# Kernel tuning notes

Measured on AMD Instinct MI355X. Metric: run time of the kernel, lower is better.

The kernel has to match this reference:

```python
import jax, jax.numpy as jnp
import numpy as np

GROUPS = 8   # channels // group_size with group_size=8 for C=64
EPS = 1e-5


def group_norm_qc(x0, x1, gamma, beta):
    """LatticeGroupNorm: stats computed jointly over both cosets per (batch, group)."""
    B, C, H, W = x0.shape
    g = GROUPS
    xg = jnp.concatenate([x0.reshape(B, g, -1), x1.reshape(B, g, -1)], axis=-1)
    mean = xg.mean(axis=-1).reshape(B, g, 1, 1, 1)
    var = xg.var(axis=-1).reshape(B, g, 1, 1, 1)
    inv = jax.lax.rsqrt(var + EPS)
    ga = gamma[None, :, None, None]
    be = beta[None, :, None, None]

    def norm(x):
        xr = x.reshape(B, g, C // g, H, W)
        return ((xr - mean) * inv).reshape(B, C, H, W) * ga + be

    return norm(x0), norm(x1)


def qc_conv(x0, x1, w_center, w_corner, bias):
    """Quincunx LatticePad+LatticeConvolution with stencil
    [(0,0),(2,0),(0,2),(2,2),(1,1)], center (1,1).
    w_center: [O,I] tap (1,1) (same-coset 1x1).
    w_corner: [O,I,2,2] taps (0,0),(2,0),(0,2),(2,2) (cross-coset 2x2).
    Pad keeps output cosets the same size as inputs ('same' lattice conv)."""
    dn = ('NCHW', 'OIHW', 'NCHW')

    def c1(x):
        return jnp.einsum('oi,bihw->bohw', w_center, x)

    def c2(x, pad):
        return jax.lax.conv_general_dilated(x, w_corner, (1, 1), pad,
                                            dimension_numbers=dn)

    b = bias[None, :, None, None]
    # coset0 output gathers coset1 at (i-1+a, j-1+b) -> pad top/left
    out0 = c1(x0) + c2(x1, ((1, 0), (1, 0))) + b
    # coset1 output gathers coset0 at (i+a, j+b) -> pad bottom/right
    out1 = c1(x1) + c2(x0, ((0, 1), (0, 1))) + b
    return out0, out1


def setup_inputs() -> dict:
    key = jax.random.key(0)
    ks = jax.random.split(key, 10)
    B, C, H, W = 2, 64, 256, 256
    s = 0.05
    return {
        'x0': jax.random.normal(ks[0], (B, C, H, W), jnp.float32),
        'x1': jax.random.normal(ks[1], (B, C, H, W), jnp.float32),
        'g1': jnp.ones((C,), jnp.float32),
        'b1': jnp.zeros((C,), jnp.float32),
        'w1_center': jax.random.normal(ks[2], (C, C), jnp.float32) * s,
        'w1_corner': jax.random.normal(ks[3], (C, C, 2, 2), jnp.float32) * s,
        'bias1': jax.random.normal(ks[4], (C,), jnp.float32) * s,
        'g2': jnp.ones((C,), jnp.float32),
        'b2': jnp.zeros((C,), jnp.float32),
        'w2_center': jax.random.normal(ks[5], (C, C), jnp.float32) * s,
        'w2_corner': jax.random.normal(ks[6], (C, C, 2, 2), jnp.float32) * s,
        'bias2': jax.random.normal(ks[7], (C,), jnp.float32) * s,
        'w_skip': jax.random.normal(ks[8], (C, C), jnp.float32) * s,
        'bias_skip': jax.random.normal(ks[9], (C,), jnp.float32) * s,
        'g_skip': jnp.ones((C,), jnp.float32),
        'beta_skip': jnp.zeros((C,), jnp.float32),
    }


def reference(x0, x1, g1, b1, w1_center, w1_corner, bias1,
              g2, b2, w2_center, w2_corner, bias2,
              w_skip, bias_skip, g_skip, beta_skip):
    # conv path: GN -> ReLU -> pad+conv -> GN -> ReLU -> pad+conv
    h0, h1 = group_norm_qc(x0, x1, g1, b1)
    h0, h1 = jax.nn.relu(h0), jax.nn.relu(h1)
    h0, h1 = qc_conv(h0, h1, w1_center, w1_corner, bias1)
    h0, h1 = group_norm_qc(h0, h1, g2, b2)
    h0, h1 = jax.nn.relu(h0), jax.nn.relu(h1)
    h0, h1 = qc_conv(h0, h1, w2_center, w2_corner, bias2)
    # skip path: 1x1 lattice conv (stencil [(0,0)]) -> GN
    bsk = bias_skip[None, :, None, None]
    s0 = jnp.einsum('oi,bihw->bohw', w_skip, x0) + bsk
    s1 = jnp.einsum('oi,bihw->bohw', w_skip, x1) + bsk
    s0, s1 = group_norm_qc(s0, s1, g_skip, beta_skip)
    # residual add; stack the two cosets as leading axis for a single output
    return jnp.stack([h0 + s0, h1 + s1])
```

## Files before the change

### kernel.cpp

```cpp
#include <hip/hip_runtime.h>

typedef __attribute__((ext_vector_type(8))) __bf16 bf16x8;
typedef __attribute__((ext_vector_type(4))) __bf16 bf16x4;
typedef __attribute__((ext_vector_type(4))) float f32x4;

#define MFMA16(a,b,c) __builtin_amdgcn_mfma_f32_16x16x32_bf16(a,b,c,0,0,0)

static constexpr int HW = 65536;
static constexpr int WD = 256;
static constexpr int NB = 2;
static constexpr double INV_N = 1.0 / 1048576.0;
static constexpr float EPSV = 1e-5f;

static constexpr size_t OFF_P1  = 0;
static constexpr size_t OFF_P2  = 131072;
static constexpr size_t OFF_A1  = 200704;
static constexpr size_t OFF_A2  = OFF_A1 + 40960;
static constexpr size_t OFF_XT  = OFF_A2 + 40960;
static constexpr size_t SZ_T    = (size_t)2 * NB * HW * 64 * 2;
static constexpr size_t OFF_S   = OFF_XT + SZ_T;
static constexpr size_t OFF_H   = OFF_S + SZ_T;

__global__ __launch_bounds__(256) void K1(
    const float* __restrict__ x0, const float* __restrict__ x1,
    const float* __restrict__ wskip, const float* __restrict__ bskip,
    const float* __restrict__ wc1, const float* __restrict__ wk1,
    const float* __restrict__ wc2, const float* __restrict__ wk2,
    __bf16* __restrict__ xt, __bf16* __restrict__ sout,
    __bf16* __restrict__ A1, __bf16* __restrict__ A2, float* __restrict__ p1) {
  const int bx = blockIdx.x;
  const int t = threadIdx.x;

  if (bx >= 1024) {
    const int stage = bx - 1024;
    const float* wc = stage ? wc2 : wc1;
    const float* wk = stage ? wk2 : wk1;
    __bf16* A = stage ? A2 : A1;
    for (int idx = t; idx < 64 * 320; idx += 256) {
      int o = idx / 320, k = idx - o * 320;
      float v;
      if (k < 64) v = wc[o * 64 + k];
      else {
        int tp = (k - 64) >> 6;
        int c = k & 63;
        v = wk[(o * 64 + c) * 4 + tp];
      }
      A[idx] = (__bf16)v;
    }
    return;
  }

  const int row = bx & 255;
  const int b   = (bx >> 8) & 1;
  const int co  = bx >> 9;
  const float* x = co ? x1 : x0;
  __shared__ __attribute__((aligned(16))) __bf16 tile[256 * 72];
  __shared__ float redp[256];
  __shared__ float reds[32];
  const int wv = t >> 6, lane = t & 63;

  const float* xbase = x + (size_t)b * 64 * HW + (size_t)row * WD + t;
  __bf16* xtbase = xt + (((size_t)(co * NB + b) * HW) + (size_t)row * WD + t) * 64;

  float gsum[8], gsq[8];
#pragma unroll
  for (int g = 0; g < 8; ++g) { gsum[g] = 0.f; gsq[g] = 0.f; }
#pragma unroll
  for (int cg = 0; cg < 8; ++cg) {
    float f[8];
#pragma unroll
    for (int j = 0; j < 8; ++j) f[j] = xbase[(size_t)(cg * 8 + j) * HW];
    bf16x8 v;
#pragma unroll
    for (int j = 0; j < 8; ++j) {
      v[j] = (__bf16)f[j];
      gsum[cg] += f[j];
      gsq[cg] = fmaf(f[j], f[j], gsq[cg]);
    }
    *(bf16x8*)&tile[t * 72 + cg * 8] = v;
    *(bf16x8*)&xtbase[cg * 8] = v;
  }
#pragma unroll
  for (int g = 0; g < 8; ++g) {
#pragma unroll
    for (int m = 1; m < 16; m <<= 1) {
      gsum[g] += __shfl_xor(gsum[g], m, 64);
      gsq[g]  += __shfl_xor(gsq[g], m, 64);
    }
  }
  {
    const int q0 = lane >> 4;
    if ((lane & 15) == 0) {
#pragma unroll
      for (int g = 0; g < 8; ++g) {
        redp[(wv * 4 + q0) * 16 + g] = gsum[g];
        redp[(wv * 4 + q0) * 16 + 8 + g] = gsq[g];
      }
    }
  }
  __syncthreads();

  const int ln = lane & 15, q = lane >> 4;
  const int ch0 = wv * 16 + q * 4;
  bf16x8 a0, a1;
#pragma unroll
  for (int j = 0; j < 8; ++j) {
    a0[j] = (__bf16)wskip[(wv * 16 + ln) * 64 + q * 8 + j];
    a1[j] = (__bf16)wskip[(wv * 16 + ln) * 64 + 32 + q * 8 + j];
  }
  float bia[4];
#pragma unroll
  for (int r = 0; r < 4; ++r) bia[r] = bskip[ch0 + r];

  float ssum = 0.f, ssq = 0.f;
  for (int n = 0; n < 16; ++n) {
    f32x4 acc = {0.f, 0.f, 0.f, 0.f};
    bf16x8 b0 = *(const bf16x8*)&tile[(n * 16 + ln) * 72 + q * 8];
    bf16x8 b1 = *(const bf16x8*)&tile[(n * 16 + ln) * 72 + 32 + q * 8];
    acc = MFMA16(a0, b0, acc);
    acc = MFMA16(a1, b1, acc);
    bf16x4 sv;
    float v[4];
#pragma unroll
    for (int r = 0; r < 4; ++r) {
      v[r] = acc[r] + bia[r];
      ssum += v[r];
      ssq = fmaf(v[r], v[r], ssq);
      sv[r] = (__bf16)v[r];
    }
    size_t sb = ((size_t)(co * NB + b) * 4096 + row * 16 + n) * 1024 + (wv * 4 + q) * 64 + ln * 4;
    *(bf16x4*)&sout[sb] = sv;
  }
#pragma unroll
  for (int m = 1; m < 16; m <<= 1) {
    ssum += __shfl_xor(ssum, m, 64);
    ssq  += __shfl_xor(ssq, m, 64);
  }
  if ((lane & 15) == 0) {
    reds[wv * 4 + q] = ssum;
    reds[16 + wv * 4 + q] = ssq;
  }

  __syncthreads();
  if (t < 32) {
    float val;
    if (t < 16) {
      val = 0.f;
#pragma unroll
      for (int k = 0; k < 16; ++k) val += redp[k * 16 + t];
    } else {
      int kind = (t >> 3) & 1, g = t & 7;
      int wvv = g >> 1, qp = g & 1;
      val = reds[kind * 16 + wvv * 4 + qp * 2] + reds[kind * 16 + wvv * 4 + qp * 2 + 1];
    }
    const int bf1 = (co * 2 + b) * 256 + row;
    p1[(size_t)bf1 * 32 + t] = val;
  }
}

__global__ __launch_bounds__(256) void K2(
    const __bf16* __restrict__ xt, const __bf16* __restrict__ A1,
    const float* __restrict__ p1, const float* __restrict__ g1, const float* __restrict__ be1,
    const float* __restrict__ bias1,
    __bf16* __restrict__ h, float* __restrict__ p2) {
  const int blk = ((blockIdx.x & 7) << 6) | (blockIdx.x >> 3);
  const int tx = blk & 15, ty = blk >> 4;
  const int b = blockIdx.y;
  const int y0p = ty * 8, x0p = tx * 16;
  __shared__ __attribute__((aligned(16))) __bf16 tl[2][153 * 72];
  __shared__ double redn[16];
  __shared__ float sc[64], sh[64];
  __shared__ float lst[16];
  const int t = threadIdx.x;

  {
    const int col = t >> 4, sub = t & 15;
    double v = 0.0;
    for (int j = sub; j < 512; j += 16) {
      int cc = j >> 8, rr = j & 255;
      v += (double)p1[((size_t)(cc * 2 + b) * 256 + rr) * 32 + col];
    }
    v += __shfl_xor(v, 1, 64);
    v += __shfl_xor(v, 2, 64);
    v += __shfl_xor(v, 4, 64);
    v += __shfl_xor(v, 8, 64);
    if (sub == 0) redn[col] = v;
  }
  if (t < 16) lst[t] = 0.f;
  __syncthreads();
  if (t < 64) {
    int g = t >> 3;
    double mean = redn[g] * INV_N;
    double var  = redn[8 + g] * INV_N - mean * mean;
    float inv = rsqrtf((float)var + EPSV);
    float s_ = inv * g1[t];
    sc[t] = s_;
    sh[t] = be1[t] - (float)mean * s_;
  }
  __syncthreads();

#pragma unroll
  for (int i = 0; i < 10; ++i) {
    int u = t + i * 256;
    if (u < 2 * 153 * 8) {
      int cs = u / 1224;
      int rr = u - cs * 1224;
      int px = rr >> 3, cg = rr & 7;
      int ly = px / 17, lx = px - ly * 17;
      int gy = y0p + ly - cs, gx = x0p + lx - cs;
      bf16x8 v;
#pragma unroll
      for (int j = 0; j < 8; ++j) v[j] = (__bf16)0.f;
      if ((unsigned)gy < 256u && (unsigned)gx < 256u) {
        bf16x8 raw = *(const bf16x8*)&xt[(((size_t)(cs * NB + b) * WD + gy) * WD + gx) * 64 + cg * 8];
#pragma unroll
        for (int j = 0; j < 8; ++j) {
          float f = fmaf((float)raw[j], sc[cg * 8 + j], sh[cg * 8 + j]);
          v[j] = (__bf16)fmaxf(f, 0.f);
        }
      }
      *(bf16x8*)&tl[cs][px * 72 + cg * 8] = v;
    }
  }
  __syncthreads();

  const int wv = t >> 6, lane = t & 63, ln = lane & 15, q = lane >> 4;
  const int co = wv & 1, mh = wv >> 1;
  const int q8 = q * 8;
  bf16x8 af[2][10];
#pragma unroll
  for (int m = 0; m < 2; ++m)
#pragma unroll
    for (int kk = 0; kk < 10; ++kk)
      af[m][kk] = *(const bf16x8*)&A1[(mh * 32 + m * 16 + ln) * 320 + kk * 32 + q8];

  f32x4 acc[8][2];
#pragma unroll
  for (int n = 0; n < 8; ++n)
#pragma unroll
    for (int m = 0; m < 2; ++m) acc[n][m] = (f32x4){0.f, 0.f, 0.f, 0.f};

  const __bf16* tc = tl[co];
  const __bf16* to = tl[1 - co];
#pragma unroll
  for (int n = 0; n < 8; ++n) {
    const int cpix = co ? ((n + 1) * 17 + ln + 1) : (n * 17 + ln);
    const int tb = n * 17 + ln;
    const __bf16* pc = tc + cpix * 72 + q8;
    const __bf16* p0 = to + tb * 72 + q8;
    const __bf16* p1p = to + (tb + 1) * 72 + q8;
    const __bf16* p2p = to + (tb + 17) * 72 + q8;
    const __bf16* p3 = to + (tb + 18) * 72 + q8;
    bf16x8 bb;
    bb = *(const bf16x8*)pc;         acc[n][0]=MFMA16(af[0][0],bb,acc[n][0]); acc[n][1]=MFMA16(af[1][0],bb,acc[n][1]);
    bb = *(const bf16x8*)(pc + 32);  acc[n][0]=MFMA16(af[0][1],bb,acc[n][0]); acc[n][1]=MFMA16(af[1][1],bb,acc[n][1]);
    bb = *(const bf16x8*)p0;         acc[n][0]=MFMA16(af[0][2],bb,acc[n][0]); acc[n][1]=MFMA16(af[1][2],bb,acc[n][1]);
    bb = *(const bf16x8*)(p0 + 32);  acc[n][0]=MFMA16(af[0][3],bb,acc[n][0]); acc[n][1]=MFMA16(af[1][3],bb,acc[n][1]);
    bb = *(const bf16x8*)p1p;        acc[n][0]=MFMA16(af[0][4],bb,acc[n][0]); acc[n][1]=MFMA16(af[1][4],bb,acc[n][1]);
    bb = *(const bf16x8*)(p1p + 32); acc[n][0]=MFMA16(af[0][5],bb,acc[n][0]); acc[n][1]=MFMA16(af[1][5],bb,acc[n][1]);
    bb = *(const bf16x8*)p2p;        acc[n][0]=MFMA16(af[0][6],bb,acc[n][0]); acc[n][1]=MFMA16(af[1][6],bb,acc[n][1]);
    bb = *(const bf16x8*)(p2p + 32); acc[n][0]=MFMA16(af[0][7],bb,acc[n][0]); acc[n][1]=MFMA16(af[1][7],bb,acc[n][1]);
    bb = *(const bf16x8*)p3;         acc[n][0]=MFMA16(af[0][8],bb,acc[n][0]); acc[n][1]=MFMA16(af[1][8],bb,acc[n][1]);
    bb = *(const bf16x8*)(p3 + 32);  acc[n][0]=MFMA16(af[0][9],bb,acc[n][0]); acc[n][1]=MFMA16(af[1][9],bb,acc[n][1]);
  }

  __syncthreads();

  float s2s[2] = {0.f, 0.f}, s2q[2] = {0.f, 0.f};
  float bia[2][4];
#pragma unroll
  for (int m = 0; m < 2; ++m)
#pragma unroll
    for (int r = 0; r < 4; ++r) bia[m][r] = bias1[mh * 32 + m * 16 + q * 4 + r];

#pragma unroll
  for (int n = 0; n < 8; ++n)
#pragma unroll
    for (int m = 0; m < 2; ++m) {
      bf16x4 hv;
#pragma unroll
      for (int r = 0; r < 4; ++r) {
        float v = acc[n][m][r] + bia[m][r];
        s2s[m] += v;
        s2q[m] = fmaf(v, v, s2q[m]);
        hv[r] = (__bf16)v;
      }
      *(bf16x4*)&tl[co][(n * 16 + ln) * 72 + mh * 32 + m * 16 + q * 4] = hv;
    }

#pragma unroll
  for (int m = 0; m < 2; ++m) {
    float a_ = s2s[m], c_ = s2q[m];
#pragma unroll
    for (int mk = 1; mk < 32; mk <<= 1) {
      a_ += __shfl_xor(a_, mk, 64);
      c_ += __shfl_xor(c_, mk, 64);
    }
    if ((lane & 31) == 0) {
      int g = mh * 4 + m * 2 + (q >> 1);
      atomicAdd(&lst[g], a_);
      atomicAdd(&lst[8 + g], c_);
    }
  }
  __syncthreads();

#pragma unroll
  for (int i = 0; i < 8; ++i) {
    int co2 = i >> 2;
    int idx = (i & 3) * 256 + t;
    int px = idx >> 3, chunk = idx & 7;
    int gy = y0p + (px >> 4), gx = x0p + (px & 15);
    bf16x8 vv = *(const bf16x8*)&tl[co2][px * 72 + chunk * 8];
    *(bf16x8*)&h[(((size_t)(co2 * NB + b) * WD + gy) * WD + gx) * 64 + chunk * 8] = vv;
  }

  if (t < 16) p2[((size_t)b * 512 + blockIdx.x) * 16 + t] = lst[t];
}

__global__ __launch_bounds__(256) void K3(
    const __bf16* __restrict__ hin, const __bf16* __restrict__ A2,
    const float* __restrict__ p2, const float* __restrict__ p1,
    const float* __restrict__ g2, const float* __restrict__ be2, const float* __restrict__ bias2,
    const float* __restrict__ gsk, const float* __restrict__ besk,
    const __bf16* __restrict__ sin_, float* __restrict__ out) {
  const int blk = ((blockIdx.x & 7) << 6) | (blockIdx.x >> 3);
  const int tx = blk & 15, ty = blk >> 4;
  const int b = blockIdx.y;
  const int y0p = ty * 8, x0p = tx * 16;
  __shared__ __attribute__((aligned(16))) __bf16 tl[2][153 * 72];
  __shared__ double redn[32];
  __shared__ float sc2[64], sh2[64], scS[64], shS[64];
  const int t = threadIdx.x;

  {
    const int col = t >> 3, sub = t & 7;
    double v = 0.0;
    if (col < 16) {
      for (int j = sub; j < 512; j += 8)
        v += (double)p2[((size_t)b * 512 + j) * 16 + col];
    } else {
      for (int j = sub; j < 512; j += 8) {
        int cc = j >> 8, rr = j & 255;
        v += (double)p1[((size_t)(cc * 2 + b) * 256 + rr) * 32 + col];
      }
    }
    v += __shfl_xor(v, 1, 64);
    v += __shfl_xor(v, 2, 64);
    v += __shfl_xor(v, 4, 64);
    if (sub == 0) redn[col] = v;
  }
  __syncthreads();
  if (t < 128) {
    int half = t >> 6, ch = t & 63, g = ch >> 3;
    if (half == 0) {
      double mean = redn[g] * INV_N;
      double var  = redn[8 + g] * INV_N - mean * mean;
      float inv = rsqrtf((float)var + EPSV);
      float s_ = inv * g2[ch];
      sc2[ch] = s_;
      sh2[ch] = be2[ch] - (float)mean * s_;
    } else {
      double mean = redn[16 + g] * INV_N;
      double var  = redn[24 + g] * INV_N - mean * mean;
      float inv = rsqrtf((float)var + EPSV);
      float s_ = inv * gsk[ch];
      scS[ch] = s_;
      shS[ch] = besk[ch] - (float)mean * s_;
    }
  }
  __syncthreads();

#pragma unroll
  for (int i = 0; i < 10; ++i) {
    int u = t + i * 256;
    if (u < 2 * 153 * 8) {
      int cs = u / 1224;
      int rr = u - cs * 1224;
      int px = rr >> 3, cg = rr & 7;
      int ly = px / 17, lx = px - ly * 17;
      int gy = y0p + ly - cs, gx = x0p + lx - cs;
      bf16x8 v;
#pragma unroll
      for (int j = 0; j < 8; ++j) v[j] = (__bf16)0.f;
      if ((unsigned)gy < 256u && (unsigned)gx < 256u) {
        bf16x8 raw = *(const bf16x8*)&hin[(((size_t)(cs * NB + b) * WD + gy) * WD + gx) * 64 + cg * 8];
#pragma unroll
        for (int j = 0; j < 8; ++j) {
          float f = fmaf((float)raw[j], sc2[cg * 8 + j], sh2[cg * 8 + j]);
          v[j] = (__bf16)fmaxf(f, 0.f);
        }
      }
      *(bf16x8*)&tl[cs][px * 72 + cg * 8] = v;
    }
  }
  __syncthreads();

  const int wv = t >> 6, lane = t & 63, ln = lane & 15, q = lane >> 4;
  const int co = wv & 1, mh = wv >> 1;
  const int q8 = q * 8;
  bf16x8 af[2][10];
#pragma unroll
  for (int m = 0; m < 2; ++m)
#pragma unroll
    for (int kk = 0; kk < 10; ++kk)
      af[m][kk] = *(const bf16x8*)&A2[(mh * 32 + m * 16 + ln) * 320 + kk * 32 + q8];

  f32x4 acc[8][2];
#pragma unroll
  for (int n = 0; n < 8; ++n)
#pragma unroll
    for (int m = 0; m < 2; ++m) acc[n][m] = (f32x4){0.f, 0.f, 0.f, 0.f};

  const __bf16* tc = tl[co];
  const __bf16* to = tl[1 - co];
#pragma unroll
  for (int n = 0; n < 8; ++n) {
    const int cpix = co ? ((n + 1) * 17 + ln + 1) : (n * 17 + ln);
    const int tb = n * 17 + ln;
    const __bf16* pc = tc + cpix * 72 + q8;
    const __bf16* p0 = to + tb * 72 + q8;
    const __bf16* p1p = to + (tb + 1) * 72 + q8;
    const __bf16* p2p = to + (tb + 17) * 72 + q8;
    const __bf16* p3 = to + (tb + 18) * 72 + q8;
    bf16x8 bb;
    bb = *(const bf16x8*)pc;         acc[n][0]=MFMA16(af[0][0],bb,acc[n][0]); acc[n][1]=MFMA16(af[1][0],bb,acc[n][1]);
    bb = *(const bf16x8*)(pc + 32);  acc[n][0]=MFMA16(af[0][1],bb,acc[n][0]); acc[n][1]=MFMA16(af[1][1],bb,acc[n][1]);
    bb = *(const bf16x8*)p0;         acc[n][0]=MFMA16(af[0][2],bb,acc[n][0]); acc[n][1]=MFMA16(af[1][2],bb,acc[n][1]);
    bb = *(const bf16x8*)(p0 + 32);  acc[n][0]=MFMA16(af[0][3],bb,acc[n][0]); acc[n][1]=MFMA16(af[1][3],bb,acc[n][1]);
    bb = *(const bf16x8*)p1p;        acc[n][0]=MFMA16(af[0][4],bb,acc[n][0]); acc[n][1]=MFMA16(af[1][4],bb,acc[n][1]);
    bb = *(const bf16x8*)(p1p + 32); acc[n][0]=MFMA16(af[0][5],bb,acc[n][0]); acc[n][1]=MFMA16(af[1][5],bb,acc[n][1]);
    bb = *(const bf16x8*)p2p;        acc[n][0]=MFMA16(af[0][6],bb,acc[n][0]); acc[n][1]=MFMA16(af[1][6],bb,acc[n][1]);
    bb = *(const bf16x8*)(p2p + 32); acc[n][0]=MFMA16(af[0][7],bb,acc[n][0]); acc[n][1]=MFMA16(af[1][7],bb,acc[n][1]);
    bb = *(const bf16x8*)p3;         acc[n][0]=MFMA16(af[0][8],bb,acc[n][0]); acc[n][1]=MFMA16(af[1][8],bb,acc[n][1]);
    bb = *(const bf16x8*)(p3 + 32);  acc[n][0]=MFMA16(af[0][9],bb,acc[n][0]); acc[n][1]=MFMA16(af[1][9],bb,acc[n][1]);
  }

  float bia[2][4], sA[2][4], sB[2][4];
#pragma unroll
  for (int m = 0; m < 2; ++m)
#pragma unroll
    for (int r = 0; r < 4; ++r) {
      int ch = mh * 32 + m * 16 + q * 4 + r;
      bia[m][r] = bias2[ch];
      sA[m][r] = scS[ch];
      sB[m][r] = shS[ch];
    }

#pragma unroll
  for (int n = 0; n < 8; ++n) {
    int gy = y0p + n;
#pragma unroll
    for (int m = 0; m < 2; ++m) {
      int ch0 = mh * 32 + m * 16 + q * 4;
      size_t sb = ((size_t)(co * NB + b) * 4096 + gy * 16 + tx) * 1024 + (mh * 8 + m * 4 + q) * 64 + ln * 4;
      bf16x4 sv = *(const bf16x4*)&sin_[sb];
      size_t ob = ((size_t)(co * NB + b) * 64 + ch0) * HW + (size_t)gy * WD + x0p + ln;
#pragma unroll
      for (int r = 0; r < 4; ++r) {
        float v = acc[n][m][r] + bia[m][r] + fmaf((float)sv[r], sA[m][r], sB[m][r]);
        out[ob + (size_t)r * HW] = v;
      }
    }
  }
}

extern "C" void kernel_launch(void* const* d_in, const int* in_sizes, int n_in,
                              void* d_out, int out_size, void* d_ws, size_t ws_size,
                              hipStream_t stream) {
  (void)in_sizes; (void)n_in; (void)out_size; (void)ws_size;
  const float* x0    = (const float*)d_in[0];
  const float* x1    = (const float*)d_in[1];
  const float* g1    = (const float*)d_in[2];
  const float* b1    = (const float*)d_in[3];
  const float* w1c   = (const float*)d_in[4];
  const float* w1k   = (const float*)d_in[5];
  const float* bias1 = (const float*)d_in[6];
  const float* g2    = (const float*)d_in[7];
  const float* b2    = (const float*)d_in[8];
  const float* w2c   = (const float*)d_in[9];
  const float* w2k   = (const float*)d_in[10];
  const float* bias2 = (const float*)d_in[11];
  const float* wsk   = (const float*)d_in[12];
  const float* bsk   = (const float*)d_in[13];
  const float* gsk   = (const float*)d_in[14];
  const float* besk  = (const float*)d_in[15];

  char* ws = (char*)d_ws;
  float*  p1 = (float*)(ws + OFF_P1);
  float*  p2 = (float*)(ws + OFF_P2);
  __bf16* A1 = (__bf16*)(ws + OFF_A1);
  __bf16* A2 = (__bf16*)(ws + OFF_A2);
  __bf16* xt = (__bf16*)(ws + OFF_XT);
  __bf16* s  = (__bf16*)(ws + OFF_S);
  __bf16* h  = (__bf16*)(ws + OFF_H);

  K1<<<dim3(1026), 256, 0, stream>>>(x0, x1, wsk, bsk, w1c, w1k, w2c, w2k, xt, s, A1, A2, p1);
  K2<<<dim3(512, 2), 256, 0, stream>>>(xt, A1, p1, g1, b1, bias1, h, p2);
  K3<<<dim3(512, 2), 256, 0, stream>>>(h, A2, p2, p1, g2, b2, bias2, gsk, besk, s, (float*)d_out);
}
```

Before: 294.7 us.

## XOR-swizzle LDS tiles, prefetch global tiles before stats, batch loads

Replaces the padded 72-stride LDS tiles with 64-stride tiles that use an XOR swizzle on the 8-element chunk index. This shrinks shared memory while still avoiding bank conflicts. K2 and K3 now issue all halo global loads into registers before computing the GroupNorm statistics, so load latency overlaps the reduction. K1 batches 32 channel loads per half, K3 batches skip-tensor loads ahead of the output stores, and all kernels get launch bounds of 4 waves/EU. The added register arrays (raw[10], f[32]) raise register pressure and could conflict with the occupancy hint.

Measured after the change: 309.1 us. 1.05x slower.

```diff
diff --git a/kernel.cpp b/kernel.cpp
--- a/kernel.cpp
+++ b/kernel.cpp
@@ -21,7 +21,9 @@
 static constexpr size_t OFF_S   = OFF_XT + SZ_T;
 static constexpr size_t OFF_H   = OFF_S + SZ_T;
 
-__global__ __launch_bounds__(256) void K1(
+#define TL8(base, px, c) (*(const bf16x8*)&(base)[(px) * 64 + (((c)) ^ ((((px)) & 7) << 3))])
+
+__global__ __launch_bounds__(256, 4) void K1(
     const float* __restrict__ x0, const float* __restrict__ x1,
     const float* __restrict__ wskip, const float* __restrict__ bskip,
     const float* __restrict__ wc1, const float* __restrict__ wk1,
@@ -54,7 +56,7 @@
   const int b   = (bx >> 8) & 1;
   const int co  = bx >> 9;
   const float* x = co ? x1 : x0;
-  __shared__ __attribute__((aligned(16))) __bf16 tile[256 * 72];
+  __shared__ __attribute__((aligned(16))) __bf16 tile[256 * 64];
   __shared__ float redp[256];
   __shared__ float reds[32];
   const int wv = t >> 6, lane = t & 63;
@@ -66,19 +68,25 @@
 #pragma unroll
   for (int g = 0; g < 8; ++g) { gsum[g] = 0.f; gsq[g] = 0.f; }
 #pragma unroll
-  for (int cg = 0; cg < 8; ++cg) {
-    float f[8];
-#pragma unroll
-    for (int j = 0; j < 8; ++j) f[j] = xbase[(size_t)(cg * 8 + j) * HW];
-    bf16x8 v;
-#pragma unroll
-    for (int j = 0; j < 8; ++j) {
-      v[j] = (__bf16)f[j];
-      gsum[cg] += f[j];
-      gsq[cg] = fmaf(f[j], f[j], gsq[cg]);
-    }
-    *(bf16x8*)&tile[t * 72 + cg * 8] = v;
-    *(bf16x8*)&xtbase[cg * 8] = v;
+  for (int hf = 0; hf < 2; ++hf) {
+    float f[32];
+#pragma unroll
+    for (int k = 0; k < 32; ++k) f[k] = xbase[(size_t)(hf * 32 + k) * HW];
+    __builtin_amdgcn_sched_barrier(0);
+#pragma unroll
+    for (int c4 = 0; c4 < 4; ++c4) {
+      const int cg = hf * 4 + c4;
+      bf16x8 v;
+#pragma unroll
+      for (int j = 0; j < 8; ++j) {
+        float xv = f[c4 * 8 + j];
+        v[j] = (__bf16)xv;
+        gsum[cg] += xv;
+        gsq[cg] = fmaf(xv, xv, gsq[cg]);
+      }
+      *(bf16x8*)&tile[t * 64 + ((cg ^ (t & 7)) * 8)] = v;
+      *(bf16x8*)&xtbase[cg * 8] = v;
+    }
   }
 #pragma unroll
   for (int g = 0; g < 8; ++g) {
@@ -115,8 +123,9 @@
   float ssum = 0.f, ssq = 0.f;
   for (int n = 0; n < 16; ++n) {
     f32x4 acc = {0.f, 0.f, 0.f, 0.f};
-    bf16x8 b0 = *(const bf16x8*)&tile[(n * 16 + ln) * 72 + q * 8];
-    bf16x8 b1 = *(const bf16x8*)&tile[(n * 16 + ln) * 72 + 32 + q * 8];
+    const int px = n * 16 + ln;
+    bf16x8 b0 = TL8(tile, px, q * 8);
+    bf16x8 b1 = TL8(tile, px, q * 8 + 32);
     acc = MFMA16(a0, b0, acc);
     acc = MFMA16(a1, b1, acc);
     bf16x4 sv;
@@ -158,7 +167,7 @@
   }
 }
 
-__global__ __launch_bounds__(256) void K2(
+__global__ __launch_bounds__(256, 4) void K2(
     const __bf16* __restrict__ xt, const __bf16* __restrict__ A1,
     const float* __restrict__ p1, const float* __restrict__ g1, const float* __restrict__ be1,
     const float* __restrict__ bias1,
@@ -167,18 +176,33 @@
   const int tx = blk & 15, ty = blk >> 4;
   const int b = blockIdx.y;
   const int y0p = ty * 8, x0p = tx * 16;
-  __shared__ __attribute__((aligned(16))) __bf16 tl[2][153 * 72];
-  __shared__ double redn[16];
+  __shared__ __attribute__((aligned(16))) __bf16 tl[2][153 * 64];
   __shared__ float sc[64], sh[64];
   __shared__ float lst[16];
+  __shared__ double redn[16];
   const int t = threadIdx.x;
 
+  bf16x8 raw[10];
+#pragma unroll
+  for (int i = 0; i < 10; ++i) {
+    int u = t + i * 256;
+    int cs = (u >= 1224) ? 1 : 0;
+    int rr = u - cs * 1224;
+    int px = rr >> 3, cg = rr & 7;
+    int ly = px / 17, lx = px - ly * 17;
+    int gy = y0p + ly - cs, gx = x0p + lx - cs;
+    if (u < 2448 && (unsigned)gy < 256u && (unsigned)gx < 256u)
+      raw[i] = *(const bf16x8*)&xt[(((size_t)(cs * NB + b) * WD + gy) * WD + gx) * 64 + cg * 8];
+  }
+  __builtin_amdgcn_sched_barrier(0);
+
+  if (t < 16) lst[t] = 0.f;
   {
     const int col = t >> 4, sub = t & 15;
     double v = 0.0;
     for (int j = sub; j < 512; j += 16) {
-      int cc = j >> 8, rr = j & 255;
-      v += (double)p1[((size_t)(cc * 2 + b) * 256 + rr) * 32 + col];
+      int cc = j >> 8, rr2 = j & 255;
+      v += (double)p1[((size_t)(cc * 2 + b) * 256 + rr2) * 32 + col];
     }
     v += __shfl_xor(v, 1, 64);
     v += __shfl_xor(v, 2, 64);
@@ -186,7 +210,6 @@
     v += __shfl_xor(v, 8, 64);
     if (sub == 0) redn[col] = v;
   }
-  if (t < 16) lst[t] = 0.f;
   __syncthreads();
   if (t < 64) {
     int g = t >> 3;
@@ -202,27 +225,22 @@
 #pragma unroll
   for (int i = 0; i < 10; ++i) {
     int u = t + i * 256;
-    if (u < 2 * 153 * 8) {
-      int cs = u / 1224;
-      int rr = u - cs * 1224;
-      int px = rr >> 3, cg = rr & 7;
-      int ly = px / 17, lx = px - ly * 17;
-      int gy = y0p + ly - cs, gx = x0p + lx - cs;
+    int cs = (u >= 1224) ? 1 : 0;
+    int rr = u - cs * 1224;
+    int px = rr >> 3, cg = rr & 7;
+    int ly = px / 17, lx = px - ly * 17;
+    int gy = y0p + ly - cs, gx = x0p + lx - cs;
+    if (u < 2448) {
+      bool inb = (unsigned)gy < 256u && (unsigned)gx < 256u;
       bf16x8 v;
 #pragma unroll
-      for (int j = 0; j < 8; ++j) v[j] = (__bf16)0.f;
-      if ((unsigned)gy < 256u && (unsigned)gx < 256u) {
-        bf16x8 raw = *(const bf16x8*)&xt[(((size_t)(cs * NB + b) * WD + gy) * WD + gx) * 64 + cg * 8];
-#pragma unroll
-        for (int j = 0; j < 8; ++j) {
-          float f = fmaf((float)raw[j], sc[cg * 8 + j], sh[cg * 8 + j]);
-          v[j] = (__bf16)fmaxf(f, 0.f);
-        }
-      }
-      *(bf16x8*)&tl[cs][px * 72 + cg * 8] = v;
-    }
-  }
-  __syncthreads();
+      for (int j = 0; j < 8; ++j) {
+        float fv = inb ? fmaf((float)raw[i][j], sc[cg * 8 + j], sh[cg * 8 + j]) : 0.f;
+        v[j] = (__bf16)fmaxf(fv, 0.f);
+      }
+      *(bf16x8*)&tl[cs][px * 64 + ((cg ^ (px & 7)) * 8)] = v;
+    }
+  }
 
   const int wv = t >> 6, lane = t & 63, ln = lane & 15, q = lane >> 4;
   const int co = wv & 1, mh = wv >> 1;
@@ -233,6 +251,7 @@
 #pragma unroll
     for (int kk = 0; kk < 10; ++kk)
       af[m][kk] = *(const bf16x8*)&A1[(mh * 32 + m * 16 + ln) * 320 + kk * 32 + q8];
+  __syncthreads();
 
   f32x4 acc[8][2];
 #pragma unroll
@@ -246,22 +265,17 @@
   for (int n = 0; n < 8; ++n) {
     const int cpix = co ? ((n + 1) * 17 + ln + 1) : (n * 17 + ln);
     const int tb = n * 17 + ln;
-    const __bf16* pc = tc + cpix * 72 + q8;
-    const __bf16* p0 = to + tb * 72 + q8;
-    const __bf16* p1p = to + (tb + 1) * 72 + q8;
-    const __bf16* p2p = to + (tb + 17) * 72 + q8;
-    const __bf16* p3 = to + (tb + 18) * 72 + q8;
     bf16x8 bb;
-    bb = *(const bf16x8*)pc;         acc[n][0]=MFMA16(af[0][0],bb,acc[n][0]); acc[n][1]=MFMA16(af[1][0],bb,acc[n][1]);
-    bb = *(const bf16x8*)(pc + 32);  acc[n][0]=MFMA16(af[0][1],bb,acc[n][0]); acc[n][1]=MFMA16(af[1][1],bb,acc[n][1]);
-    bb = *(const bf16x8*)p0;         acc[n][0]=MFMA16(af[0][2],bb,acc[n][0]); acc[n][1]=MFMA16(af[1][2],bb,acc[n][1]);
-    bb = *(const bf16x8*)(p0 + 32);  acc[n][0]=MFMA16(af[0][3],bb,acc[n][0]); acc[n][1]=MFMA16(af[1][3],bb,acc[n][1]);
-    bb = *(const bf16x8*)p1p;        acc[n][0]=MFMA16(af[0][4],bb,acc[n][0]); acc[n][1]=MFMA16(af[1][4],bb,acc[n][1]);
-    bb = *(const bf16x8*)(p1p + 32); acc[n][0]=MFMA16(af[0][5],bb,acc[n][0]); acc[n][1]=MFMA16(af[1][5],bb,acc[n][1]);
-    bb = *(const bf16x8*)p2p;        acc[n][0]=MFMA16(af[0][6],bb,acc[n][0]); acc[n][1]=MFMA16(af[1][6],bb,acc[n][1]);
-    bb = *(const bf16x8*)(p2p + 32); acc[n][0]=MFMA16(af[0][7],bb,acc[n][0]); acc[n][1]=MFMA16(af[1][7],bb,acc[n][1]);
-    bb = *(const bf16x8*)p3;         acc[n][0]=MFMA16(af[0][8],bb,acc[n][0]); acc[n][1]=MFMA16(af[1][8],bb,acc[n][1]);
-    bb = *(const bf16x8*)(p3 + 32);  acc[n][0]=MFMA16(af[0][9],bb,acc[n][0]); acc[n][1]=MFMA16(af[1][9],bb,acc[n][1]);
+    bb = TL8(tc, cpix, q8);          acc[n][0]=MFMA16(af[0][0],bb,acc[n][0]); acc[n][1]=MFMA16(af[1][0],bb,acc[n][1]);
+    bb = TL8(tc, cpix, q8 + 32);     acc[n][0]=MFMA16(af[0][1],bb,acc[n][0]); acc[n][1]=MFMA16(af[1][1],bb,acc[n][1]);
+    bb = TL8(to, tb, q8);            acc[n][0]=MFMA16(af[0][2],bb,acc[n][0]); acc[n][1]=MFMA16(af[1][2],bb,acc[n][1]);
+    bb = TL8(to, tb, q8 + 32);       acc[n][0]=MFMA16(af[0][3],bb,acc[n][0]); acc[n][1]=MFMA16(af[1][3],bb,acc[n][1]);
+    bb = TL8(to, tb + 1, q8);        acc[n][0]=MFMA16(af[0][4],bb,acc[n][0]); acc[n][1]=MFMA16(af[1][4],bb,acc[n][1]);
+    bb = TL8(to, tb + 1, q8 + 32);   acc[n][0]=MFMA16(af[0][5],bb,acc[n][0]); acc[n][1]=MFMA16(af[1][5],bb,acc[n][1]);
+    bb = TL8(to, tb + 17, q8);       acc[n][0]=MFMA16(af[0][6],bb,acc[n][0]); acc[n][1]=MFMA16(af[1][6],bb,acc[n][1]);
+    bb = TL8(to, tb + 17, q8 + 32);  acc[n][0]=MFMA16(af[0][7],bb,acc[n][0]); acc[n][1]=MFMA16(af[1][7],bb,acc[n][1]);
+    bb = TL8(to, tb + 18, q8);       acc[n][0]=MFMA16(af[0][8],bb,acc[n][0]); acc[n][1]=MFMA16(af[1][8],bb,acc[n][1]);
+    bb = TL8(to, tb + 18, q8 + 32);  acc[n][0]=MFMA16(af[0][9],bb,acc[n][0]); acc[n][1]=MFMA16(af[1][9],bb,acc[n][1]);
   }
 
   __syncthreads();
@@ -285,7 +299,7 @@
         s2q[m] = fmaf(v, v, s2q[m]);
         hv[r] = (__bf16)v;
       }
-      *(bf16x4*)&tl[co][(n * 16 + ln) * 72 + mh * 32 + m * 16 + q * 4] = hv;
+      *(bf16x4*)&tl[co][(n * 16 + ln) * 64 + ((mh * 32 + m * 16 + q * 4) ^ ((ln & 7) << 3))] = hv;
     }
 
 #pragma unroll
@@ -310,14 +324,14 @@
     int idx = (i & 3) * 256 + t;
     int px = idx >> 3, chunk = idx & 7;
     int gy = y0p + (px >> 4), gx = x0p + (px & 15);
-    bf16x8 vv = *(const bf16x8*)&tl[co2][px * 72 + chunk * 8];
+    bf16x8 vv = *(const bf16x8*)&tl[co2][px * 64 + ((chunk ^ (px & 7)) * 8)];
     *(bf16x8*)&h[(((size_t)(co2 * NB + b) * WD + gy) * WD + gx) * 64 + chunk * 8] = vv;
   }
 
   if (t < 16) p2[((size_t)b * 512 + blockIdx.x) * 16 + t] = lst[t];
 }
 
-__global__ __launch_bounds__(256) void K3(
+__global__ __launch_bounds__(256, 4) void K3(
     const __bf16* __restrict__ hin, const __bf16* __restrict__ A2,
     const float* __restrict__ p2, const float* __restrict__ p1,
     const float* __restrict__ g2, const float* __restrict__ be2, const float* __restrict__ bias2,
@@ -327,10 +341,24 @@
   const int tx = blk & 15, ty = blk >> 4;
   const int b = blockIdx.y;
   const int y0p = ty * 8, x0p = tx * 16;
-  __shared__ __attribute__((aligned(16))) __bf16 tl[2][153 * 72];
+  __shared__ __attribute__((aligned(16))) __bf16 tl[2][153 * 64];
+  __shared__ float sc2[64], sh2[64], scS[64], shS[64];
   __shared__ double redn[32];
-  __shared__ float sc2[64], sh2[64], scS[64], shS[64];
   const int t = threadIdx.x;
+
+  bf16x8 raw[10];
+#pragma unroll
+  for (int i = 0; i < 10; ++i) {
+    int u = t + i * 256;
+    int cs = (u >= 1224) ? 1 : 0;
+    int rr = u - cs * 1224;
+    int px = rr >> 3, cg = rr & 7;
+    int ly = px / 17, lx = px - ly * 17;
+    int gy = y0p + ly - cs, gx = x0p + lx - cs;
+    if (u < 2448 && (unsigned)gy < 256u && (unsigned)gx < 256u)
+      raw[i] = *(const bf16x8*)&hin[(((size_t)(cs * NB + b) * WD + gy) * WD + gx) * 64 + cg * 8];
+  }
+  __builtin_amdgcn_sched_barrier(0);
 
   {
     const int col = t >> 3, sub = t & 7;
@@ -340,8 +368,8 @@
         v += (double)p2[((size_t)b * 512 + j) * 16 + col];
     } else {
       for (int j = sub; j < 512; j += 8) {
-        int cc = j >> 8, rr = j & 255;
-        v += (double)p1[((size_t)(cc * 2 + b) * 256 + rr) * 32 + col];
+        int cc = j >> 8, rr2 = j & 255;
+        v += (double)p1[((size_t)(cc * 2 + b) * 256 + rr2) * 32 + col];
       }
     }
     v += __shfl_xor(v, 1, 64);
@@ -373,27 +401,22 @@
 #pragma unroll
   for (int i = 0; i < 10; ++i) {
     int u = t + i * 256;
-    if (u < 2 * 153 * 8) {
-      int cs = u / 1224;
-      int rr = u - cs * 1224;
-      int px = rr >> 3, cg = rr & 7;
-      int ly = px / 17, lx = px - ly * 17;
-      int gy = y0p + ly - cs, gx = x0p + lx - cs;
+    int cs = (u >= 1224) ? 1 : 0;
+    int rr = u - cs * 1224;
+    int px = rr >> 3, cg = rr & 7;
+    int ly = px / 17, lx = px - ly * 17;
+    int gy = y0p + ly - cs, gx = x0p + lx - cs;
+    if (u < 2448) {
+      bool inb = (unsigned)gy < 256u && (unsigned)gx < 256u;
       bf16x8 v;
 #pragma unroll
-      for (int j = 0; j < 8; ++j) v[j] = (__bf16)0.f;
-      if ((unsigned)gy < 256u && (unsigned)gx < 256u) {
-        bf16x8 raw = *(const bf16x8*)&hin[(((size_t)(cs * NB + b) * WD + gy) * WD + gx) * 64 + cg * 8];
-#pragma unroll
-        for (int j = 0; j < 8; ++j) {
-          float f = fmaf((float)raw[j], sc2[cg * 8 + j], sh2[cg * 8 + j]);
-          v[j] = (__bf16)fmaxf(f, 0.f);
-        }
-      }
-      *(bf16x8*)&tl[cs][px * 72 + cg * 8] = v;
-    }
-  }
-  __syncthreads();
+      for (int j = 0; j < 8; ++j) {
+        float fv = inb ? fmaf((float)raw[i][j], sc2[cg * 8 + j], sh2[cg * 8 + j]) : 0.f;
+        v[j] = (__bf16)fmaxf(fv, 0.f);
+      }
+      *(bf16x8*)&tl[cs][px * 64 + ((cg ^ (px & 7)) * 8)] = v;
+    }
+  }
 
   const int wv = t >> 6, lane = t & 63, ln = lane & 15, q = lane >> 4;
   const int co = wv & 1, mh = wv >> 1;
@@ -404,6 +427,7 @@
 #pragma unroll
     for (int kk = 0; kk < 10; ++kk)
       af[m][kk] = *(const bf16x8*)&A2[(mh * 32 + m * 16 + ln) * 320 + kk * 32 + q8];
+  __syncthreads();
 
   f32x4 acc[8][2];
 #pragma unroll
@@ -417,22 +441,17 @@
   for (int n = 0; n < 8; ++n) {
     const int cpix = co ? ((n + 1) * 17 + ln + 1) : (n * 17 + ln);
     const int tb = n * 17 + ln;
-    const __bf16* pc = tc + cpix * 72 + q8;
-    const __bf16* p0 = to + tb * 72 + q8;
-    const __bf16* p1p = to + (tb + 1) * 72 + q8;
-    const __bf16* p2p = to + (tb + 17) * 72 + q8;
-    const __bf16* p3 = to + (tb + 18) * 72 + q8;
     bf16x8 bb;
-    bb = *(const bf16x8*)pc;         acc[n][0]=MFMA16(af[0][0],bb,acc[n][0]); acc[n][1]=MFMA16(af[1][0],bb,acc[n][1]);
-    bb = *(const bf16x8*)(pc + 32);  acc[n][0]=MFMA16(af[0][1],bb,acc[n][0]); acc[n][1]=MFMA16(af[1][1],bb,acc[n][1]);
-    bb = *(const bf16x8*)p0;         acc[n][0]=MFMA16(af[0][2],bb,acc[n][0]); acc[n][1]=MFMA16(af[1][2],bb,acc[n][1]);
-    bb = *(const bf16x8*)(p0 + 32);  acc[n][0]=MFMA16(af[0][3],bb,acc[n][0]); acc[n][1]=MFMA16(af[1][3],bb,acc[n][1]);
-    bb = *(const bf16x8*)p1p;        acc[n][0]=MFMA16(af[0][4],bb,acc[n][0]); acc[n][1]=MFMA16(af[1][4],bb,acc[n][1]);
-    bb = *(const bf16x8*)(p1p + 32); acc[n][0]=MFMA16(af[0][5],bb,acc[n][0]); acc[n][1]=MFMA16(af[1][5],bb,acc[n][1]);
-    bb = *(const bf16x8*)p2p;        acc[n][0]=MFMA16(af[0][6],bb,acc[n][0]); acc[n][1]=MFMA16(af[1][6],bb,acc[n][1]);
-    bb = *(const bf16x8*)(p2p + 32); acc[n][0]=MFMA16(af[0][7],bb,acc[n][0]); acc[n][1]=MFMA16(af[1][7],bb,acc[n][1]);
-    bb = *(const bf16x8*)p3;         acc[n][0]=MFMA16(af[0][8],bb,acc[n][0]); acc[n][1]=MFMA16(af[1][8],bb,acc[n][1]);
-    bb = *(const bf16x8*)(p3 + 32);  acc[n][0]=MFMA16(af[0][9],bb,acc[n][0]); acc[n][1]=MFMA16(af[1][9],bb,acc[n][1]);
+    bb = TL8(tc, cpix, q8);          acc[n][0]=MFMA16(af[0][0],bb,acc[n][0]); acc[n][1]=MFMA16(af[1][0],bb,acc[n][1]);
+    bb = TL8(tc, cpix, q8 + 32);     acc[n][0]=MFMA16(af[0][1],bb,acc[n][0]); acc[n][1]=MFMA16(af[1][1],bb,acc[n][1]);
+    bb = TL8(to, tb, q8);            acc[n][0]=MFMA16(af[0][2],bb,acc[n][0]); acc[n][1]=MFMA16(af[1][2],bb,acc[n][1]);
+    bb = TL8(to, tb, q8 + 32);       acc[n][0]=MFMA16(af[0][3],bb,acc[n][0]); acc[n][1]=MFMA16(af[1][3],bb,acc[n][1]);
+    bb = TL8(to, tb + 1, q8);        acc[n][0]=MFMA16(af[0][4],bb,acc[n][0]); acc[n][1]=MFMA16(af[1][4],bb,acc[n][1]);
+    bb = TL8(to, tb + 1, q8 + 32);   acc[n][0]=MFMA16(af[0][5],bb,acc[n][0]); acc[n][1]=MFMA16(af[1][5],bb,acc[n][1]);
+    bb = TL8(to, tb + 17, q8);       acc[n][0]=MFMA16(af[0][6],bb,acc[n][0]); acc[n][1]=MFMA16(af[1][6],bb,acc[n][1]);
+    bb = TL8(to, tb + 17, q8 + 32);  acc[n][0]=MFMA16(af[0][7],bb,acc[n][0]); acc[n][1]=MFMA16(af[1][7],bb,acc[n][1]);
+    bb = TL8(to, tb + 18, q8);       acc[n][0]=MFMA16(af[0][8],bb,acc[n][0]); acc[n][1]=MFMA16(af[1][8],bb,acc[n][1]);
+    bb = TL8(to, tb + 18, q8 + 32);  acc[n][0]=MFMA16(af[0][9],bb,acc[n][0]); acc[n][1]=MFMA16(af[1][9],bb,acc[n][1]);
   }
 
   float bia[2][4], sA[2][4], sB[2][4];
@@ -447,18 +466,30 @@
     }
 
 #pragma unroll
-  for (int n = 0; n < 8; ++n) {
-    int gy = y0p + n;
-#pragma unroll
-    for (int m = 0; m < 2; ++m) {
-      int ch0 = mh * 32 + m * 16 + q * 4;
-      size_t sb = ((size_t)(co * NB + b) * 4096 + gy * 16 + tx) * 1024 + (mh * 8 + m * 4 + q) * 64 + ln * 4;
-      bf16x4 sv = *(const bf16x4*)&sin_[sb];
-      size_t ob = ((size_t)(co * NB + b) * 64 + ch0) * HW + (size_t)gy * WD + x0p + ln;
-#pragma unroll
-      for (int r = 0; r < 4; ++r) {
-        float v = acc[n][m][r] + bia[m][r] + fmaf((float)sv[r], sA[m][r], sB[m][r]);
-        out[ob + (size_t)r * HW] = v;
+  for (int ng = 0; ng < 2; ++ng) {
+    bf16x4 sv[4][2];
+#pragma unroll
+    for (int nn = 0; nn < 4; ++nn) {
+      int n = ng * 4 + nn;
+      int gy = y0p + n;
+#pragma unroll
+      for (int m = 0; m < 2; ++m)
+        sv[nn][m] = *(const bf16x4*)&sin_[((size_t)(co * NB + b) * 4096 + gy * 16 + tx) * 1024 + (mh * 8 + m * 4 + q) * 64 + ln * 4];
+    }
+    __builtin_amdgcn_sched_barrier(0);
+#pragma unroll
+    for (int nn = 0; nn < 4; ++nn) {
+      int n = ng * 4 + nn;
+      int gy = y0p + n;
+#pragma unroll
+      for (int m = 0; m < 2; ++m) {
+        int ch0 = mh * 32 + m * 16 + q * 4;
+        size_t ob = ((size_t)(co * NB + b) * 64 + ch0) * HW + (size_t)gy * WD + x0p + ln;
+#pragma unroll
+        for (int r = 0; r < 4; ++r) {
+          float v = acc[n][m][r] + bia[m][r] + fmaf((float)sv[nn][m][r], sA[m][r], sB[m][r]);
+          out[ob + (size_t)r * HW] = v;
+        }
       }
     }
   }
```
